# Optimization experiments

Hardware: AMD Instinct MI355X
Metric: run time of the kernel (lower is better)

## Reference

```python
import jax, jax.numpy as jnp
import numpy as np

B, S, V, H = 256, 512, 768, 50


def setup_inputs() -> dict:
    key = jax.random.key(0)
    ks = jax.random.split(key, 5)
    sc = 1.0 / np.sqrt(V)
    return {
        "output_1": jax.random.normal(ks[0], (B, S, V), dtype=jnp.float32),
        "output_2": jax.random.normal(ks[1], (B, S, V), dtype=jnp.float32),
        "Wg": jax.random.normal(ks[2], (H, 2 * V), dtype=jnp.float32) * sc,
        "bg": jnp.zeros((H,), dtype=jnp.float32),
        "Wfd": jax.random.normal(ks[3], (H, 2 * H), dtype=jnp.float32) * 0.1,
        "bfd": jnp.zeros((H,), dtype=jnp.float32),
        "Wff": jax.random.normal(ks[4], (1, H), dtype=jnp.float32) * 0.1,
        "bff": jnp.zeros((1,), dtype=jnp.float32),
    }


def reference(output_1, output_2, Wg, bg, Wfd, bfd, Wff, bff):
    # Append doc-mean sentence: [B, S+1, V]
    x1 = jnp.concatenate([output_1, jnp.mean(output_1, axis=1, keepdims=True)], axis=1)
    x2 = jnp.concatenate([output_2, jnp.mean(output_2, axis=1, keepdims=True)], axis=1)

    # Bidirectional cross-attention scores: a[b, s, t] = <x1[b,s], x2[b,t]>
    a = jnp.einsum('bsv,btv->bst', x1, x2)
    a_x = jax.nn.softmax(a, axis=1)   # softmax over x1's sentence axis
    a_y = jax.nn.softmax(a, axis=0)   # softmax over the BATCH axis (as in the original)

    attention_x = jnp.einsum('bst,bsv->btv', a_x, x1)  # [B, S+1, V]
    attention_y = jnp.einsum('bst,btv->bsv', a_y, x2)  # [B, S+1, V]

    out_x = jnp.concatenate([x1, attention_y], axis=2) @ Wg.T + bg  # [B, S+1, H]
    out_y = jnp.concatenate([x2, attention_x], axis=2) @ Wg.T + bg

    # Training branch: take the doc-mean (last) position
    o1 = out_x[:, -1, :]  # [B, H]
    o2 = out_y[:, -1, :]
    h = jax.nn.relu(jnp.concatenate([o1, o2], axis=1) @ Wfd.T + bfd)  # [B, H]
    logit = jnp.squeeze(h @ Wff.T + bff)  # [B]
    return jax.nn.sigmoid(logit)
```

## Files before the change

kernel.cpp:

```cpp
#include <hip/hip_runtime.h>
#include <math.h>

#define BB 256
#define SS 512
#define VV 768
#define TT 513
#define HH 50

#define OFF_M1    0
#define OFF_M2    (OFF_M1 + BB*VV)
#define OFF_XPART (OFF_M2 + BB*VV)
#define XPART_STRIDE 772
#define OFF_AROW  (OFF_XPART + 4*BB*XPART_STRIDE)
#define AROW_STRIDE 520
#define OFF_COLM  (OFF_AROW + BB*AROW_STRIDE)
#define OFF_COLRD (OFF_COLM + 520)
#define OFF_YPART (OFF_COLRD + 520)

__global__ __launch_bounds__(192) void k_mean1(const float* __restrict__ o1,
                                               float* __restrict__ ws) {
    int bid   = blockIdx.x;
    int chunk = bid & 7;
    int b     = bid >> 3;
    float* dst = ws + OFF_M1 + b * VV;
    int tid = threadIdx.x;
    const float4* p = (const float4*)(o1 + (size_t)b * SS * VV + (size_t)chunk * 64 * VV) + tid;
    float4 acc = {0.f, 0.f, 0.f, 0.f};
#pragma unroll 4
    for (int s = 0; s < 64; ++s) {
        float4 x = p[(size_t)s * 192];
        acc.x += x.x; acc.y += x.y; acc.z += x.z; acc.w += x.w;
    }
    const float inv = 1.0f / 512.0f;
    float* d4 = dst + tid * 4;
    atomicAdd(d4 + 0, acc.x * inv);
    atomicAdd(d4 + 1, acc.y * inv);
    atomicAdd(d4 + 2, acc.z * inv);
    atomicAdd(d4 + 3, acc.w * inv);
}

__global__ __launch_bounds__(256) void k_o2fused(const float* __restrict__ o2,
                                                 float* __restrict__ ws) {
    int bid = blockIdx.x;
    int tc = bid & 7, b = bid >> 3;
    int tid = threadIdx.x, wave = tid >> 6, lane = tid & 63;
    const float4* m14 = (const float4*)(ws + OFF_M1 + b * VV);
    float4 mf0 = m14[lane], mf1 = m14[lane + 64], mf2 = m14[lane + 128];
    const float* base = o2 + (size_t)b * SS * VV;
    float* arow = ws + OFF_AROW + b * AROW_STRIDE;
    float4 s0 = {0,0,0,0}, s1 = {0,0,0,0}, s2 = {0,0,0,0};
    int t0 = tc * 64 + wave * 16;
#pragma unroll 2
    for (int i = 0; i < 16; ++i) {
        int t = t0 + i;
        const float4* r4 = (const float4*)(base + (size_t)t * VV);
        float4 x0 = r4[lane], x1 = r4[lane + 64], x2 = r4[lane + 128];
        s0.x += x0.x; s0.y += x0.y; s0.z += x0.z; s0.w += x0.w;
        s1.x += x1.x; s1.y += x1.y; s1.z += x1.z; s1.w += x1.w;
        s2.x += x2.x; s2.y += x2.y; s2.z += x2.z; s2.w += x2.w;
        float p = x0.x*mf0.x + x0.y*mf0.y + x0.z*mf0.z + x0.w*mf0.w
                + x1.x*mf1.x + x1.y*mf1.y + x1.z*mf1.z + x1.w*mf1.w
                + x2.x*mf2.x + x2.y*mf2.y + x2.z*mf2.z + x2.w*mf2.w;
#pragma unroll
        for (int off = 32; off > 0; off >>= 1) p += __shfl_down(p, off);
        if (lane == 0) arow[t] = p;
    }
    __shared__ __align__(16) float red[4][VV];
    float4* my4 = (float4*)red[wave];
    my4[lane] = s0; my4[lane + 64] = s1; my4[lane + 128] = s2;
    __syncthreads();
    const float inv = 1.0f / 512.0f;
#pragma unroll
    for (int j = 0; j < 3; ++j) {
        int col = tid + 256 * j;
        float s = red[0][col] + red[1][col] + red[2][col] + red[3][col];
        atomicAdd(ws + OFF_M2 + b * VV + col, s * inv);
    }
}

__global__ __launch_bounds__(64) void k_vrow(float* __restrict__ ws) {
    int b = blockIdx.x, lane = threadIdx.x;
    const float4* m14 = (const float4*)(ws + OFF_M1 + b * VV);
    const float4* m24 = (const float4*)(ws + OFF_M2 + b * VV);
    float p = 0.f;
#pragma unroll
    for (int k = 0; k < 3; ++k) {
        float4 a = m14[lane + 64 * k], c = m24[lane + 64 * k];
        p += a.x*c.x + a.y*c.y + a.z*c.z + a.w*c.w;
    }
#pragma unroll
    for (int off = 32; off > 0; off >>= 1) p += __shfl_down(p, off);
    if (lane == 0) ws[OFF_AROW + b * AROW_STRIDE + SS] = p;
}

__global__ __launch_bounds__(256) void k_colstats(float* __restrict__ ws) {
    int t = blockIdx.x;
    int tid = threadIdx.x;
    int wave = tid >> 6, lane = tid & 63;
    float v = ws[OFF_AROW + tid * AROW_STRIDE + t];
    __shared__ float red[4], red2[4];
    float m = v;
#pragma unroll
    for (int off = 32; off > 0; off >>= 1) m = fmaxf(m, __shfl_down(m, off));
    if (lane == 0) red[wave] = m;
    __syncthreads();
    float m0 = fmaxf(fmaxf(red[0], red[1]), fmaxf(red[2], red[3]));
    float e = __expf(v - m0);
#pragma unroll
    for (int off = 32; off > 0; off >>= 1) e += __shfl_down(e, off);
    if (lane == 0) red2[wave] = e;
    __syncthreads();
    if (tid == 0) {
        float D = red2[0] + red2[1] + red2[2] + red2[3];
        ws[OFF_COLM + t]  = m0;
        ws[OFF_COLRD + t] = 1.0f / D;
    }
}

#define XCHUNK 8
__global__ __launch_bounds__(256) void k_xside(const float* __restrict__ o1,
                                               float* __restrict__ ws) {
    int part = blockIdx.x & 3;
    int b    = blockIdx.x >> 2;
    int tid  = threadIdx.x;
    int wave = tid >> 6, lane = tid & 63;
    __shared__ __align__(16) float tile[XCHUNK][VV];
    __shared__ float sc[XCHUNK];

    const float4* m24 = (const float4*)(ws + OFF_M2 + b * VV);
    float4 mf0 = m24[lane], mf1 = m24[lane + 64], mf2 = m24[lane + 128];

    int s0 = part * 128;
    const float4* base4 = (const float4*)(o1 + (size_t)b * SS * VV + (size_t)s0 * VV);

    float4 r0 = base4[tid],        r1 = base4[256 + tid],  r2 = base4[512 + tid],
           r3 = base4[768 + tid],  r4 = base4[1024 + tid], r5 = base4[1280 + tid];

    float accv0 = 0.f, accv1 = 0.f, accv2 = 0.f;
    float M = -1e30f, d = 0.f;

    for (int c = 0; c < 128 / XCHUNK; ++c) {
        float4* l4 = (float4*)&tile[0][0];
        l4[tid] = r0; l4[256 + tid] = r1; l4[512 + tid] = r2;
        l4[768 + tid] = r3; l4[1024 + tid] = r4; l4[1280 + tid] = r5;
        if (c < 128 / XCHUNK - 1) {
            const float4* g = base4 + (size_t)(c + 1) * (XCHUNK * VV / 4);
            r0 = g[tid]; r1 = g[256 + tid]; r2 = g[512 + tid];
            r3 = g[768 + tid]; r4 = g[1024 + tid]; r5 = g[1280 + tid];
        }
        __syncthreads();
#pragma unroll
        for (int r2i = 0; r2i < 2; ++r2i) {
            int row = wave * 2 + r2i;
            const float4* trow = (const float4*)&tile[row][0];
            float4 a0 = trow[lane], a1 = trow[lane + 64], a2 = trow[lane + 128];
            float p = a0.x*mf0.x + a0.y*mf0.y + a0.z*mf0.z + a0.w*mf0.w
                    + a1.x*mf1.x + a1.y*mf1.y + a1.z*mf1.z + a1.w*mf1.w
                    + a2.x*mf2.x + a2.y*mf2.y + a2.z*mf2.z + a2.w*mf2.w;
#pragma unroll
            for (int off = 32; off > 0; off >>= 1) p += __shfl_down(p, off);
            if (lane == 0) sc[row] = p;
        }
        __syncthreads();
        float sv[XCHUNK], cmax = -1e30f;
#pragma unroll
        for (int j = 0; j < XCHUNK; ++j) { sv[j] = sc[j]; cmax = fmaxf(cmax, sv[j]); }
        float newM  = fmaxf(M, cmax);
        float scale = __expf(M - newM);
        float w[XCHUNK], wsum = 0.f;
#pragma unroll
        for (int j = 0; j < XCHUNK; ++j) { w[j] = __expf(sv[j] - newM); wsum += w[j]; }
        d = d * scale + wsum;
        {
            float a0 = accv0 * scale, a1 = accv1 * scale, a2 = accv2 * scale;
#pragma unroll
            for (int j = 0; j < XCHUNK; ++j) {
                a0 += w[j] * tile[j][tid];
                a1 += w[j] * tile[j][tid + 256];
                a2 += w[j] * tile[j][tid + 512];
            }
            accv0 = a0; accv1 = a1; accv2 = a2;
        }
        M = newM;
        __syncthreads();
    }

    if (part == 3) {
        const float* m1p = ws + OFF_M1 + b * VV;
        for (int i = tid; i < VV; i += 256) tile[0][i] = m1p[i];
        __syncthreads();
        if (wave == 0) {
            const float4* trow = (const float4*)&tile[0][0];
            float4 a0 = trow[lane], a1 = trow[lane + 64], a2 = trow[lane + 128];
            float p = a0.x*mf0.x + a0.y*mf0.y + a0.z*mf0.z + a0.w*mf0.w
                    + a1.x*mf1.x + a1.y*mf1.y + a1.z*mf1.z + a1.w*mf1.w
                    + a2.x*mf2.x + a2.y*mf2.y + a2.z*mf2.z + a2.w*mf2.w;
#pragma unroll
            for (int off = 32; off > 0; off >>= 1) p += __shfl_down(p, off);
            if (lane == 0) sc[0] = p;
        }
        __syncthreads();
        float s0v   = sc[0];
        float newM  = fmaxf(M, s0v);
        float scale = __expf(M - newM);
        float w0    = __expf(s0v - newM);
        d = d * scale + w0;
        accv0 = accv0 * scale + w0 * tile[0][tid];
        accv1 = accv1 * scale + w0 * tile[0][tid + 256];
        accv2 = accv2 * scale + w0 * tile[0][tid + 512];
        M = newM;
    }

    float* outp = ws + OFF_XPART + (size_t)(part * BB + b) * XPART_STRIDE;
    outp[tid] = accv0; outp[tid + 256] = accv1; outp[tid + 512] = accv2;
    if (tid == 0) { outp[768] = M; outp[769] = d; }
}

__global__ __launch_bounds__(192) void k_yweight(const float* __restrict__ o2,
                                                 float* __restrict__ ws) {
    int part = blockIdx.x & 3, b = blockIdx.x >> 2;
    int tid = threadIdx.x;
    __shared__ float wl[129];
    int t0 = part * 128;
    const float* arow = ws + OFF_AROW + b * AROW_STRIDE;
    for (int i = tid; i < 129; i += 192) {
        if (i < 128) {
            int t = t0 + i;
            wl[i] = __expf(arow[t] - ws[OFF_COLM + t]) * ws[OFF_COLRD + t];
        } else if (part == 3) {
            wl[128] = __expf(arow[SS] - ws[OFF_COLM + SS]) * ws[OFF_COLRD + SS];
        }
    }
    __syncthreads();
    const float4* base = (const float4*)(o2 + (size_t)b * SS * VV) + tid;
    float4 acc = {0.f, 0.f, 0.f, 0.f};
#pragma unroll 4
    for (int i = 0; i < 128; ++i) {
        float w = wl[i];
        float4 x = base[(size_t)(t0 + i) * 192];
        acc.x += w * x.x; acc.y += w * x.y; acc.z += w * x.z; acc.w += w * x.w;
    }
    if (part == 3) {
        float w = wl[128];
        float4 x = ((const float4*)(ws + OFF_M2 + b * VV))[tid];
        acc.x += w * x.x; acc.y += w * x.y; acc.z += w * x.z; acc.w += w * x.w;
    }
    ((float4*)(ws + OFF_YPART + (size_t)(part * BB + b) * VV))[tid] = acc;
}

__global__ __launch_bounds__(256) void k_epilogue(const float* __restrict__ Wg,
                                                  const float* __restrict__ bg,
                                                  const float* __restrict__ Wfd,
                                                  const float* __restrict__ bfd,
                                                  const float* __restrict__ Wff,
                                                  const float* __restrict__ bff,
                                                  float* __restrict__ ws,
                                                  float* __restrict__ out) {
    int b = blockIdx.x;
    int tid = threadIdx.x;
    __shared__ __align__(16) float cx[2 * VV];
    __shared__ __align__(16) float cy[2 * VV];
    __shared__ float od[2][HH][2];
    __shared__ float o1s[HH], o2s[HH];

    float Mp[4], dp[4];
#pragma unroll
    for (int p = 0; p < 4; ++p) {
        const float* xp = ws + OFF_XPART + (size_t)(p * BB + b) * XPART_STRIDE;
        Mp[p] = xp[768];
        dp[p] = xp[769];
    }
    float M = fmaxf(fmaxf(Mp[0], Mp[1]), fmaxf(Mp[2], Mp[3]));
    float e[4], den = 0.f;
#pragma unroll
    for (int p = 0; p < 4; ++p) { e[p] = __expf(Mp[p] - M); den += dp[p] * e[p]; }
    float rden = 1.0f / den;

    for (int i = tid; i < VV; i += 256) {
        cx[i] = ws[OFF_M1 + b * VV + i];
        cy[i] = ws[OFF_M2 + b * VV + i];
        float ay = 0.f;
#pragma unroll
        for (int p = 0; p < 4; ++p) ay += ws[OFF_YPART + (size_t)(p * BB + b) * VV + i];
        cx[VV + i] = ay;
        float ax = 0.f;
#pragma unroll
        for (int p = 0; p < 4; ++p) ax += ws[OFF_XPART + (size_t)(p * BB + b) * XPART_STRIDE + i] * e[p];
        cy[VV + i] = ax * rden;
    }
    __syncthreads();

    if (tid < 200) {
        int which = tid / 100, r = tid % 100, h = r >> 1, seg = r & 1;
        const float* c = which ? cy : cx;
        const float4* cc = (const float4*)(c + seg * VV);
        const float4* wg = (const float4*)(Wg + (size_t)h * 2 * VV + seg * VV);
        float acc = 0.f;
        for (int j = 0; j < VV / 4; ++j) {
            float4 a4 = cc[j]; float4 w4 = wg[j];
            acc += a4.x * w4.x + a4.y * w4.y + a4.z * w4.z + a4.w * w4.w;
        }
        od[which][h][seg] = acc;
    }
    __syncthreads();
    if (tid < HH)                     o1s[tid]      = od[0][tid][0]    + od[0][tid][1]    + bg[tid];
    else if (tid >= 64 && tid < 64 + HH) { int h = tid - 64; o2s[h] = od[1][h][0] + od[1][h][1] + bg[h]; }
    __syncthreads();
    if (tid < 64) {
        float hv = 0.f;
        if (tid < HH) {
            float a = bfd[tid];
            for (int k = 0; k < HH; ++k)
                a += o1s[k] * Wfd[tid * 2 * HH + k] + o2s[k] * Wfd[tid * 2 * HH + HH + k];
            hv = fmaxf(a, 0.f) * Wff[tid];
        }
#pragma unroll
        for (int off = 32; off > 0; off >>= 1) hv += __shfl_down(hv, off);
        if (tid == 0) out[b] = 1.0f / (1.0f + __expf(-(hv + bff[0])));
    }
}

extern "C" void kernel_launch(void* const* d_in, const int* in_sizes, int n_in,
                              void* d_out, int out_size, void* d_ws, size_t ws_size,
                              hipStream_t stream) {
    const float* o1  = (const float*)d_in[0];
    const float* o2  = (const float*)d_in[1];
    const float* Wg  = (const float*)d_in[2];
    const float* bg  = (const float*)d_in[3];
    const float* Wfd = (const float*)d_in[4];
    const float* bfd = (const float*)d_in[5];
    const float* Wff = (const float*)d_in[6];
    const float* bff = (const float*)d_in[7];
    float* out = (float*)d_out;
    float* ws  = (float*)d_ws;

    hipMemsetAsync(ws, 0, (size_t)2 * BB * VV * sizeof(float), stream);

    k_mean1   <<<2048, 192, 0, stream>>>(o1, ws);
    k_o2fused <<<2048, 256, 0, stream>>>(o2, ws);
    k_vrow    <<< 256,  64, 0, stream>>>(ws);
    k_colstats<<< 513, 256, 0, stream>>>(ws);
    k_xside   <<<1024, 256, 0, stream>>>(o1, ws);
    k_yweight <<<1024, 192, 0, stream>>>(o2, ws);
    k_epilogue<<< 256, 256, 0, stream>>>(Wg, bg, Wfd, bfd, Wff, bff, ws, out);
}
```

Baseline: 936.2 us.

## Replace atomic mean accumulation with partial buffers and double xside/yweight split

Column means of both inputs are now written as per-chunk partial sums to separate workspace slices instead of being accumulated with atomics. This removes the memset and the atomic traffic. Partials are summed where the means are consumed, and k_vrow now also materialises the full m2 mean. The x-side and y-weight kernels are split into 8 parts per batch instead of 4, giving more blocks and more parallelism, while the epilogue merges 8 partials and some loops get unroll pragmas. The cost is extra partial reads in downstream kernels and more workspace.

```diff
diff --git a/kernel.cpp b/kernel.cpp
--- a/kernel.cpp
+++ b/kernel.cpp
@@ -4,39 +4,34 @@
 #define BB 256
 #define SS 512
 #define VV 768
-#define TT 513
 #define HH 50
 
-#define OFF_M1    0
-#define OFF_M2    (OFF_M1 + BB*VV)
+#define OFF_M1P   0
+#define OFF_M2P   (OFF_M1P + 4*BB*VV)
+#define OFF_M2    (OFF_M2P + 8*BB*VV)
 #define OFF_XPART (OFF_M2 + BB*VV)
 #define XPART_STRIDE 772
-#define OFF_AROW  (OFF_XPART + 4*BB*XPART_STRIDE)
+#define OFF_AROW  (OFF_XPART + 8*BB*XPART_STRIDE)
 #define AROW_STRIDE 520
 #define OFF_COLM  (OFF_AROW + BB*AROW_STRIDE)
 #define OFF_COLRD (OFF_COLM + 520)
 #define OFF_YPART (OFF_COLRD + 520)
 
-__global__ __launch_bounds__(192) void k_mean1(const float* __restrict__ o1,
-                                               float* __restrict__ ws) {
-    int bid   = blockIdx.x;
-    int chunk = bid & 7;
-    int b     = bid >> 3;
-    float* dst = ws + OFF_M1 + b * VV;
-    int tid = threadIdx.x;
-    const float4* p = (const float4*)(o1 + (size_t)b * SS * VV + (size_t)chunk * 64 * VV) + tid;
+__global__ __launch_bounds__(192) void k_mean1p(const float* __restrict__ o1,
+                                                float* __restrict__ ws) {
+    int chunk = blockIdx.x & 3;
+    int b     = blockIdx.x >> 2;
+    int tid   = threadIdx.x;
+    const float4* p = (const float4*)(o1 + (size_t)b * SS * VV + (size_t)chunk * 128 * VV) + tid;
     float4 acc = {0.f, 0.f, 0.f, 0.f};
-#pragma unroll 4
-    for (int s = 0; s < 64; ++s) {
+#pragma unroll 8
+    for (int s = 0; s < 128; ++s) {
         float4 x = p[(size_t)s * 192];
         acc.x += x.x; acc.y += x.y; acc.z += x.z; acc.w += x.w;
     }
     const float inv = 1.0f / 512.0f;
-    float* d4 = dst + tid * 4;
-    atomicAdd(d4 + 0, acc.x * inv);
-    atomicAdd(d4 + 1, acc.y * inv);
-    atomicAdd(d4 + 2, acc.z * inv);
-    atomicAdd(d4 + 3, acc.w * inv);
+    float4 o; o.x = acc.x * inv; o.y = acc.y * inv; o.z = acc.z * inv; o.w = acc.w * inv;
+    ((float4*)(ws + OFF_M1P + (size_t)(chunk * BB + b) * VV))[tid] = o;
 }
 
 __global__ __launch_bounds__(256) void k_o2fused(const float* __restrict__ o2,
@@ -44,8 +39,15 @@
     int bid = blockIdx.x;
     int tc = bid & 7, b = bid >> 3;
     int tid = threadIdx.x, wave = tid >> 6, lane = tid & 63;
-    const float4* m14 = (const float4*)(ws + OFF_M1 + b * VV);
-    float4 mf0 = m14[lane], mf1 = m14[lane + 64], mf2 = m14[lane + 128];
+    float4 mf0 = {0,0,0,0}, mf1 = {0,0,0,0}, mf2 = {0,0,0,0};
+#pragma unroll
+    for (int p = 0; p < 4; ++p) {
+        const float4* mp = (const float4*)(ws + OFF_M1P + (size_t)(p * BB + b) * VV);
+        float4 a = mp[lane], c = mp[lane + 64], d = mp[lane + 128];
+        mf0.x += a.x; mf0.y += a.y; mf0.z += a.z; mf0.w += a.w;
+        mf1.x += c.x; mf1.y += c.y; mf1.z += c.z; mf1.w += c.w;
+        mf2.x += d.x; mf2.y += d.y; mf2.z += d.z; mf2.w += d.w;
+    }
     const float* base = o2 + (size_t)b * SS * VV;
     float* arow = ws + OFF_AROW + b * AROW_STRIDE;
     float4 s0 = {0,0,0,0}, s1 = {0,0,0,0}, s2 = {0,0,0,0};
@@ -70,27 +72,38 @@
     my4[lane] = s0; my4[lane + 64] = s1; my4[lane + 128] = s2;
     __syncthreads();
     const float inv = 1.0f / 512.0f;
+    float* dst = ws + OFF_M2P + (size_t)(tc * BB + b) * VV;
 #pragma unroll
     for (int j = 0; j < 3; ++j) {
         int col = tid + 256 * j;
         float s = red[0][col] + red[1][col] + red[2][col] + red[3][col];
-        atomicAdd(ws + OFF_M2 + b * VV + col, s * inv);
-    }
-}
-
-__global__ __launch_bounds__(64) void k_vrow(float* __restrict__ ws) {
-    int b = blockIdx.x, lane = threadIdx.x;
-    const float4* m14 = (const float4*)(ws + OFF_M1 + b * VV);
-    const float4* m24 = (const float4*)(ws + OFF_M2 + b * VV);
-    float p = 0.f;
-#pragma unroll
-    for (int k = 0; k < 3; ++k) {
-        float4 a = m14[lane + 64 * k], c = m24[lane + 64 * k];
-        p += a.x*c.x + a.y*c.y + a.z*c.z + a.w*c.w;
-    }
+        dst[col] = s * inv;
+    }
+}
+
+__global__ __launch_bounds__(192) void k_vrow(float* __restrict__ ws) {
+    int b = blockIdx.x, tid = threadIdx.x;
+    int wave = tid >> 6, lane = tid & 63;
+    float4 m2v = {0,0,0,0};
+#pragma unroll
+    for (int p = 0; p < 8; ++p) {
+        float4 x = ((const float4*)(ws + OFF_M2P + (size_t)(p * BB + b) * VV))[tid];
+        m2v.x += x.x; m2v.y += x.y; m2v.z += x.z; m2v.w += x.w;
+    }
+    ((float4*)(ws + OFF_M2 + (size_t)b * VV))[tid] = m2v;
+    float4 m1v = {0,0,0,0};
+#pragma unroll
+    for (int p = 0; p < 4; ++p) {
+        float4 x = ((const float4*)(ws + OFF_M1P + (size_t)(p * BB + b) * VV))[tid];
+        m1v.x += x.x; m1v.y += x.y; m1v.z += x.z; m1v.w += x.w;
+    }
+    float p = m1v.x*m2v.x + m1v.y*m2v.y + m1v.z*m2v.z + m1v.w*m2v.w;
 #pragma unroll
     for (int off = 32; off > 0; off >>= 1) p += __shfl_down(p, off);
-    if (lane == 0) ws[OFF_AROW + b * AROW_STRIDE + SS] = p;
+    __shared__ float r[3];
+    if (lane == 0) r[wave] = p;
+    __syncthreads();
+    if (tid == 0) ws[OFF_AROW + b * AROW_STRIDE + SS] = r[0] + r[1] + r[2];
 }
 
 __global__ __launch_bounds__(256) void k_colstats(float* __restrict__ ws) {
@@ -120,17 +133,17 @@
 #define XCHUNK 8
 __global__ __launch_bounds__(256) void k_xside(const float* __restrict__ o1,
                                                float* __restrict__ ws) {
-    int part = blockIdx.x & 3;
-    int b    = blockIdx.x >> 2;
+    int part = blockIdx.x & 7;
+    int b    = blockIdx.x >> 3;
     int tid  = threadIdx.x;
     int wave = tid >> 6, lane = tid & 63;
     __shared__ __align__(16) float tile[XCHUNK][VV];
     __shared__ float sc[XCHUNK];
 
-    const float4* m24 = (const float4*)(ws + OFF_M2 + b * VV);
+    const float4* m24 = (const float4*)(ws + OFF_M2 + (size_t)b * VV);
     float4 mf0 = m24[lane], mf1 = m24[lane + 64], mf2 = m24[lane + 128];
 
-    int s0 = part * 128;
+    int s0 = part * 64;
     const float4* base4 = (const float4*)(o1 + (size_t)b * SS * VV + (size_t)s0 * VV);
 
     float4 r0 = base4[tid],        r1 = base4[256 + tid],  r2 = base4[512 + tid],
@@ -139,11 +152,11 @@
     float accv0 = 0.f, accv1 = 0.f, accv2 = 0.f;
     float M = -1e30f, d = 0.f;
 
-    for (int c = 0; c < 128 / XCHUNK; ++c) {
+    for (int c = 0; c < 64 / XCHUNK; ++c) {
         float4* l4 = (float4*)&tile[0][0];
         l4[tid] = r0; l4[256 + tid] = r1; l4[512 + tid] = r2;
         l4[768 + tid] = r3; l4[1024 + tid] = r4; l4[1280 + tid] = r5;
-        if (c < 128 / XCHUNK - 1) {
+        if (c < 64 / XCHUNK - 1) {
             const float4* g = base4 + (size_t)(c + 1) * (XCHUNK * VV / 4);
             r0 = g[tid]; r1 = g[256 + tid]; r2 = g[512 + tid];
             r3 = g[768 + tid]; r4 = g[1024 + tid]; r5 = g[1280 + tid];
@@ -185,9 +198,13 @@
         __syncthreads();
     }
 
-    if (part == 3) {
-        const float* m1p = ws + OFF_M1 + b * VV;
-        for (int i = tid; i < VV; i += 256) tile[0][i] = m1p[i];
+    if (part == 7) {
+        for (int i = tid; i < VV; i += 256) {
+            float s = 0.f;
+#pragma unroll
+            for (int p = 0; p < 4; ++p) s += ws[OFF_M1P + (size_t)(p * BB + b) * VV + i];
+            tile[0][i] = s;
+        }
         __syncthreads();
         if (wave == 0) {
             const float4* trow = (const float4*)&tile[0][0];
@@ -218,31 +235,31 @@
 
 __global__ __launch_bounds__(192) void k_yweight(const float* __restrict__ o2,
                                                  float* __restrict__ ws) {
-    int part = blockIdx.x & 3, b = blockIdx.x >> 2;
+    int part = blockIdx.x & 7, b = blockIdx.x >> 3;
     int tid = threadIdx.x;
-    __shared__ float wl[129];
-    int t0 = part * 128;
+    __shared__ float wl[65];
+    int t0 = part * 64;
     const float* arow = ws + OFF_AROW + b * AROW_STRIDE;
-    for (int i = tid; i < 129; i += 192) {
-        if (i < 128) {
+    for (int i = tid; i < 65; i += 192) {
+        if (i < 64) {
             int t = t0 + i;
             wl[i] = __expf(arow[t] - ws[OFF_COLM + t]) * ws[OFF_COLRD + t];
-        } else if (part == 3) {
-            wl[128] = __expf(arow[SS] - ws[OFF_COLM + SS]) * ws[OFF_COLRD + SS];
+        } else if (part == 7) {
+            wl[64] = __expf(arow[SS] - ws[OFF_COLM + SS]) * ws[OFF_COLRD + SS];
         }
     }
     __syncthreads();
     const float4* base = (const float4*)(o2 + (size_t)b * SS * VV) + tid;
     float4 acc = {0.f, 0.f, 0.f, 0.f};
 #pragma unroll 4
-    for (int i = 0; i < 128; ++i) {
+    for (int i = 0; i < 64; ++i) {
         float w = wl[i];
         float4 x = base[(size_t)(t0 + i) * 192];
         acc.x += w * x.x; acc.y += w * x.y; acc.z += w * x.z; acc.w += w * x.w;
     }
-    if (part == 3) {
-        float w = wl[128];
-        float4 x = ((const float4*)(ws + OFF_M2 + b * VV))[tid];
+    if (part == 7) {
+        float w = wl[64];
+        float4 x = ((const float4*)(ws + OFF_M2 + (size_t)b * VV))[tid];
         acc.x += w * x.x; acc.y += w * x.y; acc.z += w * x.z; acc.w += w * x.w;
     }
     ((float4*)(ws + OFF_YPART + (size_t)(part * BB + b) * VV))[tid] = acc;
@@ -263,29 +280,34 @@
     __shared__ float od[2][HH][2];
     __shared__ float o1s[HH], o2s[HH];
 
-    float Mp[4], dp[4];
-#pragma unroll
-    for (int p = 0; p < 4; ++p) {
+    float Mp[8], dp[8];
+#pragma unroll
+    for (int p = 0; p < 8; ++p) {
         const float* xp = ws + OFF_XPART + (size_t)(p * BB + b) * XPART_STRIDE;
         Mp[p] = xp[768];
         dp[p] = xp[769];
     }
-    float M = fmaxf(fmaxf(Mp[0], Mp[1]), fmaxf(Mp[2], Mp[3]));
-    float e[4], den = 0.f;
-#pragma unroll
-    for (int p = 0; p < 4; ++p) { e[p] = __expf(Mp[p] - M); den += dp[p] * e[p]; }
+    float M = -1e30f;
+#pragma unroll
+    for (int p = 0; p < 8; ++p) M = fmaxf(M, Mp[p]);
+    float e[8], den = 0.f;
+#pragma unroll
+    for (int p = 0; p < 8; ++p) { e[p] = __expf(Mp[p] - M); den += dp[p] * e[p]; }
     float rden = 1.0f / den;
 
     for (int i = tid; i < VV; i += 256) {
-        cx[i] = ws[OFF_M1 + b * VV + i];
-        cy[i] = ws[OFF_M2 + b * VV + i];
+        float m1 = 0.f;
+#pragma unroll
+        for (int p = 0; p < 4; ++p) m1 += ws[OFF_M1P + (size_t)(p * BB + b) * VV + i];
+        cx[i] = m1;
+        cy[i] = ws[OFF_M2 + (size_t)b * VV + i];
         float ay = 0.f;
 #pragma unroll
-        for (int p = 0; p < 4; ++p) ay += ws[OFF_YPART + (size_t)(p * BB + b) * VV + i];
+        for (int p = 0; p < 8; ++p) ay += ws[OFF_YPART + (size_t)(p * BB + b) * VV + i];
         cx[VV + i] = ay;
         float ax = 0.f;
 #pragma unroll
-        for (int p = 0; p < 4; ++p) ax += ws[OFF_XPART + (size_t)(p * BB + b) * XPART_STRIDE + i] * e[p];
+        for (int p = 0; p < 8; ++p) ax += ws[OFF_XPART + (size_t)(p * BB + b) * XPART_STRIDE + i] * e[p];
         cy[VV + i] = ax * rden;
     }
     __syncthreads();
@@ -296,6 +318,7 @@
         const float4* cc = (const float4*)(c + seg * VV);
         const float4* wg = (const float4*)(Wg + (size_t)h * 2 * VV + seg * VV);
         float acc = 0.f;
+#pragma unroll 4
         for (int j = 0; j < VV / 4; ++j) {
             float4 a4 = cc[j]; float4 w4 = wg[j];
             acc += a4.x * w4.x + a4.y * w4.y + a4.z * w4.z + a4.w * w4.w;
@@ -310,6 +333,7 @@
         float hv = 0.f;
         if (tid < HH) {
             float a = bfd[tid];
+#pragma unroll 5
             for (int k = 0; k < HH; ++k)
                 a += o1s[k] * Wfd[tid * 2 * HH + k] + o2s[k] * Wfd[tid * 2 * HH + HH + k];
             hv = fmaxf(a, 0.f) * Wff[tid];
@@ -334,13 +358,11 @@
     float* out = (float*)d_out;
     float* ws  = (float*)d_ws;
 
-    hipMemsetAsync(ws, 0, (size_t)2 * BB * VV * sizeof(float), stream);
-
-    k_mean1   <<<2048, 192, 0, stream>>>(o1, ws);
+    k_mean1p  <<<1024, 192, 0, stream>>>(o1, ws);
     k_o2fused <<<2048, 256, 0, stream>>>(o2, ws);
-    k_vrow    <<< 256,  64, 0, stream>>>(ws);
+    k_vrow    <<< 256, 192, 0, stream>>>(ws);
     k_colstats<<< 513, 256, 0, stream>>>(ws);
-    k_xside   <<<1024, 256, 0, stream>>>(o1, ws);
-    k_yweight <<<1024, 192, 0, stream>>>(o2, ws);
+    k_xside   <<<2048, 256, 0, stream>>>(o1, ws);
+    k_yweight <<<2048, 192, 0, stream>>>(o2, ws);
     k_epilogue<<< 256, 256, 0, stream>>>(Wg, bg, Wfd, bfd, Wff, bff, ws, out);
 }
```

Result: no change. 951.7 us (+1.7%).
